# Kernel optimization log

Measured on AMD Instinct MI355X. Metric: run time of the kernel, lower is better.

## Reference

```python
import jax, jax.numpy as jnp
import numpy as np

INPUT_DIM = 2048
N_EXPERTS = 64
K = 2


def setup_inputs() -> dict:
    key = jax.random.key(0)
    kx, kw, kb = jax.random.split(key, 3)
    x = jax.random.normal(kx, (4, 4096, INPUT_DIM), dtype=jnp.float32)
    # nn.Linear(input_dim, n_experts): weight [n_experts, input_dim], bias [n_experts]
    bound = 1.0 / np.sqrt(INPUT_DIM)
    W = jax.random.uniform(kw, (N_EXPERTS, INPUT_DIM), minval=-bound, maxval=bound, dtype=jnp.float32)
    b = jax.random.uniform(kb, (N_EXPERTS,), minval=-bound, maxval=bound, dtype=jnp.float32)
    return {"x": x, "W": W, "b": b}


def reference(x, W, b):
    # logits: [B, S, E]
    logits = jnp.einsum('bsd,ed->bse', x, W) + b
    topk_vals, topk_indices = jax.lax.top_k(logits, K)  # over last (expert) axis
    gate_probs = jax.nn.softmax(topk_vals, axis=-1)
    return gate_probs, topk_indices
```

## Files before the change

kernel.cpp:

```cpp
#include <hip/hip_runtime.h>
#include <math.h>
#include <stdint.h>

typedef _Float16 half8 __attribute__((ext_vector_type(8)));
typedef float floatx4 __attribute__((ext_vector_type(4)));

#define NTOK   16384
#define DIM    2048
#define NEXP   64
#define TPB    16
#define NBLK   (NTOK / TPB)
#define NCHW   8
#define WSW_H8 16384
#define WSW_BYTES (2 * WSW_H8 * 16)

#define ABUF_BYTES 32768
#define RED_STRIDE 68
#define RED_F      (4 * 16 * RED_STRIDE)

__global__ void wprep_kernel(const float* __restrict__ W, _Float16* __restrict__ wsw) {
    const int id   = blockIdx.x * blockDim.x + threadIdx.x;
    const int lane = id & 63;
    const int tg   = (id >> 6) & 3;
    const int sg   = id >> 8;
    const int e    = tg * 16 + (lane & 15);
    const int k    = sg * 32 + (lane >> 4) * 8;
    const float* src = W + (size_t)e * DIM + k;
    half8 h, l;
#pragma unroll
    for (int j = 0; j < 8; j++) {
        const float v  = src[j];
        const _Float16 hh = (_Float16)v;
        h[j] = hh;
        l[j] = (_Float16)((v - (float)hh) * 2048.0f);
    }
    const size_t slot = (size_t)(sg * 4 + tg) * 64 + lane;
    ((half8*)wsw)[slot]          = h;
    ((half8*)wsw)[WSW_H8 + slot] = l;
}

__device__ __forceinline__ void split_a(const float4& v0, const float4& v1,
                                        half8& hi, half8& lo) {
    const float av[8] = {v0.x, v0.y, v0.z, v0.w, v1.x, v1.y, v1.z, v1.w};
#pragma unroll
    for (int j = 0; j < 8; j++) {
        const _Float16 hh = (_Float16)av[j];
        hi[j] = hh;
        lo[j] = (_Float16)((av[j] - (float)hh) * 2048.0f);
    }
}

__device__ __forceinline__ void dma16(const void* g, const char* l) {
    __builtin_amdgcn_global_load_lds(
        (const __attribute__((address_space(1))) unsigned int*)(uintptr_t)g,
        (__attribute__((address_space(3))) unsigned int*)(uintptr_t)l,
        16, 0, 0);
}

template <bool USE_WS> struct BFrag;
template <> struct BFrag<true>  { half8  h[2][4]; half8 l[2][4]; };
template <> struct BFrag<false> { float4 a[2][4][2]; };

template <bool USE_WS>
__device__ __forceinline__ void load_b(BFrag<USE_WS>& bf, const half8* wb,
                                       const float* Wb, int cc) {
    if constexpr (USE_WS) {
#pragma unroll
        for (int s = 0; s < 2; s++)
#pragma unroll
            for (int t = 0; t < 4; t++) {
                const size_t o = (size_t)(cc * 8 + s * 4 + t) * 64;
                bf.h[s][t] = wb[o];
                bf.l[s][t] = wb[o + WSW_H8];
            }
    } else {
#pragma unroll
        for (int s = 0; s < 2; s++)
#pragma unroll
            for (int t = 0; t < 4; t++) {
                const float* wr = Wb + (size_t)(t * 16) * DIM + cc * 64 + s * 32;
                bf.a[s][t][0] = *(const float4*)wr;
                bf.a[s][t][1] = *(const float4*)(wr + 4);
            }
    }
}

template <bool USE_WS>
__global__ __launch_bounds__(256, 3)
void gating_kernel(const float* __restrict__ x, const float* __restrict__ W,
                   const _Float16* __restrict__ wsw, const float* __restrict__ bias,
                   float* __restrict__ out)
{
    __shared__ char  abuf[ABUF_BYTES];
    __shared__ float red[RED_F];

    const int tid  = threadIdx.x;
    const int lane = tid & 63;
    const int ks   = tid >> 6;
    const int col  = lane & 15;
    const int quad = lane >> 4;
    const int tok0 = blockIdx.x * TPB;

    const float* gA[4];
#pragma unroll
    for (int i = 0; i < 4; i++) {
        const int row = i * 4 + quad;
        const int pz  = col;
        const int gp  = (pz & 8) | ((pz & 7) ^ (row & 7));
        gA[i] = x + (size_t)(tok0 + row) * DIM + ks * (NCHW * 64) + gp * 4;
    }
    char* const ab = abuf + ks * 8192;
    const half8* wb = (const half8*)wsw + (size_t)ks * 4096 + lane;
    const float* Wb = W + (size_t)col * DIM + ks * (NCHW * 64) + quad * 8;

    floatx4 accm[4] = {{0,0,0,0},{0,0,0,0},{0,0,0,0},{0,0,0,0}};
    floatx4 accl[4] = {{0,0,0,0},{0,0,0,0},{0,0,0,0},{0,0,0,0}};

#pragma unroll
    for (int i = 0; i < 4; i++) dma16(gA[i], ab + i * 1024);
    asm volatile("" ::: "memory");
    BFrag<USE_WS> bc;
    load_b<USE_WS>(bc, wb, Wb, 0);
#pragma unroll
    for (int i = 0; i < 4; i++) dma16(gA[i] + 64, ab + 4096 + i * 1024);

#pragma unroll
    for (int cc = 0; cc < NCHW; ++cc) {
        if (cc == NCHW - 1) asm volatile("s_waitcnt vmcnt(16)" ::: "memory");
        else                asm volatile("s_waitcnt vmcnt(20)" ::: "memory");
        const char* Ab = ab + (cc & 1) * 4096;
        float4 v0[2], v1[2];
#pragma unroll
        for (int s = 0; s < 2; s++) {
            v0[s] = *(const float4*)(Ab + col * 256 + (8 * s + ((2 * quad + 0) ^ (col & 7))) * 16);
            v1[s] = *(const float4*)(Ab + col * 256 + (8 * s + ((2 * quad + 1) ^ (col & 7))) * 16);
        }
        asm volatile("s_waitcnt lgkmcnt(0)" ::: "memory");
        BFrag<USE_WS> bn;
        if (cc + 1 < NCHW) load_b<USE_WS>(bn, wb, Wb, cc + 1);
        if (cc + 2 < NCHW) {
#pragma unroll
            for (int i = 0; i < 4; i++)
                dma16(gA[i] + (size_t)(cc + 2) * 64, ab + (cc & 1) * 4096 + i * 1024);
        }
#pragma unroll
        for (int s = 0; s < 2; s++) {
            half8 ah, al;
            split_a(v0[s], v1[s], ah, al);
#pragma unroll
            for (int t = 0; t < 4; t++) {
                half8 bh, bl;
                if constexpr (USE_WS) {
                    bh = bc.h[s][t];
                    bl = bc.l[s][t];
                } else {
                    split_a(bc.a[s][t][0], bc.a[s][t][1], bh, bl);
                }
                accm[t] = __builtin_amdgcn_mfma_f32_16x16x32_f16(ah, bh, accm[t], 0, 0, 0);
                accl[t] = __builtin_amdgcn_mfma_f32_16x16x32_f16(ah, bl, accl[t], 0, 0, 0);
                accl[t] = __builtin_amdgcn_mfma_f32_16x16x32_f16(al, bh, accl[t], 0, 0, 0);
            }
        }
        if (cc + 1 < NCHW) bc = bn;
    }

    const float inv = 1.0f / 2048.0f;
#pragma unroll
    for (int t = 0; t < 4; t++)
#pragma unroll
        for (int r = 0; r < 4; r++)
            red[(ks * 16 + quad * 4 + r) * RED_STRIDE + t * 16 + col] =
                accm[t][r] + accl[t][r] * inv;
    __syncthreads();

    if (tid < TPB) {
        const int tk = tid;
        float v0 = -INFINITY, v1 = -INFINITY;
        int   i0 = 0, i1 = 0;
        for (int e = 0; e < NEXP; e++) {
            const float v = red[(0 * 16 + tk) * RED_STRIDE + e]
                          + red[(1 * 16 + tk) * RED_STRIDE + e]
                          + red[(2 * 16 + tk) * RED_STRIDE + e]
                          + red[(3 * 16 + tk) * RED_STRIDE + e] + bias[e];
            if (v > v0)      { v1 = v0; i1 = i0; v0 = v; i0 = e; }
            else if (v > v1) { v1 = v; i1 = e; }
        }
        const float e1 = expf(v1 - v0);
        const float sden = 1.f + e1;
        const int   g  = tok0 + tk;
        out[2 * g + 0] = 1.f / sden;
        out[2 * g + 1] = e1 / sden;
        out[2 * NTOK + 2 * g + 0] = (float)i0;
        out[2 * NTOK + 2 * g + 1] = (float)i1;
    }
}

extern "C" void kernel_launch(void* const* d_in, const int* in_sizes, int n_in,
                              void* d_out, int out_size, void* d_ws, size_t ws_size,
                              hipStream_t stream) {
    const float* x    = (const float*)d_in[0];
    const float* W    = (const float*)d_in[1];
    const float* bias = (const float*)d_in[2];
    float*       out  = (float*)d_out;
    _Float16*    wsw  = (_Float16*)d_ws;

    if (ws_size >= (size_t)WSW_BYTES) {
        hipLaunchKernelGGL(wprep_kernel, dim3(64), dim3(256), 0, stream, W, wsw);
        hipLaunchKernelGGL((gating_kernel<true>), dim3(NBLK), dim3(256), 0, stream,
                           x, W, wsw, bias, out);
    } else {
        hipLaunchKernelGGL((gating_kernel<false>), dim3(NBLK), dim3(256), 0, stream,
                           x, W, wsw, bias, out);
    }
}
```

Baseline: 211.1 us.

## Process 64 tokens per block with 8-way K split to reuse weight fragments

```diff
diff --git a/kernel.cpp b/kernel.cpp
--- a/kernel.cpp
+++ b/kernel.cpp
@@ -5,18 +5,21 @@
 typedef _Float16 half8 __attribute__((ext_vector_type(8)));
 typedef float floatx4 __attribute__((ext_vector_type(4)));
 
-#define NTOK   16384
-#define DIM    2048
-#define NEXP   64
-#define TPB    16
-#define NBLK   (NTOK / TPB)
-#define NCHW   8
+#define NTOK 16384
+#define DIM  2048
+#define NEXP 64
+#define MB   64
+#define NBLK (NTOK / MB)
+#define KSPL 8
+#define KW   (DIM / KSPL)
+#define NCH  (KW / 32)
 #define WSW_H8 16384
 #define WSW_BYTES (2 * WSW_H8 * 16)
 
-#define ABUF_BYTES 32768
-#define RED_STRIDE 68
-#define RED_F      (4 * 16 * RED_STRIDE)
+#define SLOT_B  8192
+#define WAVE_B  (2 * SLOT_B)
+#define ARING_B (8 * WAVE_B)
+#define FIN_F   (64 * 65)
 
 __global__ void wprep_kernel(const float* __restrict__ W, _Float16* __restrict__ wsw) {
     const int id   = blockIdx.x * blockDim.x + threadIdx.x;
@@ -57,131 +60,134 @@
         16, 0, 0);
 }
 
-template <bool USE_WS> struct BFrag;
-template <> struct BFrag<true>  { half8  h[2][4]; half8 l[2][4]; };
-template <> struct BFrag<false> { float4 a[2][4][2]; };
+template <int N>
+__device__ __forceinline__ void wait_vm() {
+    asm volatile("s_waitcnt vmcnt(%0)" :: "n"(N) : "memory");
+}
 
 template <bool USE_WS>
-__device__ __forceinline__ void load_b(BFrag<USE_WS>& bf, const half8* wb,
-                                       const float* Wb, int cc) {
-    if constexpr (USE_WS) {
-#pragma unroll
-        for (int s = 0; s < 2; s++)
-#pragma unroll
-            for (int t = 0; t < 4; t++) {
-                const size_t o = (size_t)(cc * 8 + s * 4 + t) * 64;
-                bf.h[s][t] = wb[o];
-                bf.l[s][t] = wb[o + WSW_H8];
-            }
-    } else {
-#pragma unroll
-        for (int s = 0; s < 2; s++)
-#pragma unroll
-            for (int t = 0; t < 4; t++) {
-                const float* wr = Wb + (size_t)(t * 16) * DIM + cc * 64 + s * 32;
-                bf.a[s][t][0] = *(const float4*)wr;
-                bf.a[s][t][1] = *(const float4*)(wr + 4);
-            }
-    }
-}
-
-template <bool USE_WS>
-__global__ __launch_bounds__(256, 3)
+__global__ __launch_bounds__(512, 2)
 void gating_kernel(const float* __restrict__ x, const float* __restrict__ W,
                    const _Float16* __restrict__ wsw, const float* __restrict__ bias,
                    float* __restrict__ out)
 {
-    __shared__ char  abuf[ABUF_BYTES];
-    __shared__ float red[RED_F];
+    __shared__ char  aring[ARING_B];
+    __shared__ float fin[FIN_F];
+    __shared__ float bsh[NEXP];
 
     const int tid  = threadIdx.x;
     const int lane = tid & 63;
     const int ks   = tid >> 6;
     const int col  = lane & 15;
     const int quad = lane >> 4;
-    const int tok0 = blockIdx.x * TPB;
-
-    const float* gA[4];
-#pragma unroll
-    for (int i = 0; i < 4; i++) {
-        const int row = i * 4 + quad;
-        const int pz  = col;
-        const int gp  = (pz & 8) | ((pz & 7) ^ (row & 7));
-        gA[i] = x + (size_t)(tok0 + row) * DIM + ks * (NCHW * 64) + gp * 4;
-    }
-    char* const ab = abuf + ks * 8192;
-    const half8* wb = (const half8*)wsw + (size_t)ks * 4096 + lane;
-    const float* Wb = W + (size_t)col * DIM + ks * (NCHW * 64) + quad * 8;
-
-    floatx4 accm[4] = {{0,0,0,0},{0,0,0,0},{0,0,0,0},{0,0,0,0}};
-    floatx4 accl[4] = {{0,0,0,0},{0,0,0,0},{0,0,0,0},{0,0,0,0}};
-
-#pragma unroll
-    for (int i = 0; i < 4; i++) dma16(gA[i], ab + i * 1024);
-    asm volatile("" ::: "memory");
-    BFrag<USE_WS> bc;
-    load_b<USE_WS>(bc, wb, Wb, 0);
-#pragma unroll
-    for (int i = 0; i < 4; i++) dma16(gA[i] + 64, ab + 4096 + i * 1024);
-
-#pragma unroll
-    for (int cc = 0; cc < NCHW; ++cc) {
-        if (cc == NCHW - 1) asm volatile("s_waitcnt vmcnt(16)" ::: "memory");
-        else                asm volatile("s_waitcnt vmcnt(20)" ::: "memory");
-        const char* Ab = ab + (cc & 1) * 4096;
-        float4 v0[2], v1[2];
-#pragma unroll
-        for (int s = 0; s < 2; s++) {
-            v0[s] = *(const float4*)(Ab + col * 256 + (8 * s + ((2 * quad + 0) ^ (col & 7))) * 16);
-            v1[s] = *(const float4*)(Ab + col * 256 + (8 * s + ((2 * quad + 1) ^ (col & 7))) * 16);
-        }
-        asm volatile("s_waitcnt lgkmcnt(0)" ::: "memory");
-        BFrag<USE_WS> bn;
-        if (cc + 1 < NCHW) load_b<USE_WS>(bn, wb, Wb, cc + 1);
-        if (cc + 2 < NCHW) {
-#pragma unroll
-            for (int i = 0; i < 4; i++)
-                dma16(gA[i] + (size_t)(cc + 2) * 64, ab + (cc & 1) * 4096 + i * 1024);
-        }
-#pragma unroll
-        for (int s = 0; s < 2; s++) {
+    const int tok0 = blockIdx.x * MB;
+
+    if (tid < NEXP) bsh[tid] = bias[tid];
+
+    const int arow = lane >> 3;
+    const int agp  = (lane & 7) ^ arow;
+    const float* gA = x + (size_t)(tok0 + arow) * DIM + ks * KW + agp * 4;
+    char* const wbase = aring + ks * WAVE_B;
+
+    floatx4 accm[4][4], accl[4][4];
+#pragma unroll
+    for (int m = 0; m < 4; m++)
+#pragma unroll
+        for (int t = 0; t < 4; t++) { accm[m][t] = (floatx4){0,0,0,0}; accl[m][t] = (floatx4){0,0,0,0}; }
+
+#pragma unroll
+    for (int i = 0; i < 8; i++)
+        dma16(gA + (size_t)i * 8 * DIM, wbase + i * 1024);
+
+#pragma unroll
+    for (int c = 0; c < NCH; ++c) {
+        const int sg = ks * NCH + c;
+        half8  bh[4], bl[4];
+        float4 bf0[4], bf1[4];
+        if constexpr (USE_WS) {
+#pragma unroll
+            for (int t = 0; t < 4; t++) {
+                bh[t] = ((const half8*)wsw)[(size_t)(sg * 4 + t) * 64 + lane];
+                bl[t] = ((const half8*)wsw)[WSW_H8 + (size_t)(sg * 4 + t) * 64 + lane];
+            }
+        } else {
+#pragma unroll
+            for (int t = 0; t < 4; t++) {
+                const float* wr = W + (size_t)(t * 16 + col) * DIM + sg * 32 + quad * 8;
+                bf0[t] = *(const float4*)wr;
+                bf1[t] = *(const float4*)(wr + 4);
+            }
+        }
+        asm volatile("" ::: "memory");
+        if (c + 1 < NCH) {
+#pragma unroll
+            for (int i = 0; i < 8; i++)
+                dma16(gA + (size_t)i * 8 * DIM + (c + 1) * 32,
+                      wbase + ((c + 1) & 1) * SLOT_B + i * 1024);
+        }
+        asm volatile("" ::: "memory");
+        if (c + 1 < NCH) wait_vm<16>();
+        else             wait_vm<8>();
+        asm volatile("" ::: "memory");
+
+        const char* Ab = wbase + (c & 1) * SLOT_B;
+#pragma unroll
+        for (int m = 0; m < 4; m++) {
+            const int row = m * 16 + col;
+            const float4 v0 = *(const float4*)(Ab + row * 128 + (((2 * quad + 0) ^ (col & 7))) * 16);
+            const float4 v1 = *(const float4*)(Ab + row * 128 + (((2 * quad + 1) ^ (col & 7))) * 16);
             half8 ah, al;
-            split_a(v0[s], v1[s], ah, al);
+            split_a(v0, v1, ah, al);
 #pragma unroll
             for (int t = 0; t < 4; t++) {
-                half8 bh, bl;
-                if constexpr (USE_WS) {
-                    bh = bc.h[s][t];
-                    bl = bc.l[s][t];
-                } else {
-                    split_a(bc.a[s][t][0], bc.a[s][t][1], bh, bl);
-                }
-                accm[t] = __builtin_amdgcn_mfma_f32_16x16x32_f16(ah, bh, accm[t], 0, 0, 0);
-                accl[t] = __builtin_amdgcn_mfma_f32_16x16x32_f16(ah, bl, accl[t], 0, 0, 0);
-                accl[t] = __builtin_amdgcn_mfma_f32_16x16x32_f16(al, bh, accl[t], 0, 0, 0);
+                half8 hb, lb;
+                if constexpr (USE_WS) { hb = bh[t]; lb = bl[t]; }
+                else                  { split_a(bf0[t], bf1[t], hb, lb); }
+                accm[m][t] = __builtin_amdgcn_mfma_f32_16x16x32_f16(ah, hb, accm[m][t], 0, 0, 0);
+                accl[m][t] = __builtin_amdgcn_mfma_f32_16x16x32_f16(ah, lb, accl[m][t], 0, 0, 0);
+                accl[m][t] = __builtin_amdgcn_mfma_f32_16x16x32_f16(al, hb, accl[m][t], 0, 0, 0);
             }
         }
-        if (cc + 1 < NCHW) bc = bn;
-    }
-
-    const float inv = 1.0f / 2048.0f;
-#pragma unroll
-    for (int t = 0; t < 4; t++)
-#pragma unroll
-        for (int r = 0; r < 4; r++)
-            red[(ks * 16 + quad * 4 + r) * RED_STRIDE + t * 16 + col] =
-                accm[t][r] + accl[t][r] * inv;
+    }
+
     __syncthreads();
-
-    if (tid < TPB) {
+    {
+        float* slab = (float*)(aring + ks * 16384);
+        const float inv = 1.0f / 2048.0f;
+#pragma unroll
+        for (int m = 0; m < 4; m++)
+#pragma unroll
+            for (int t = 0; t < 4; t++)
+#pragma unroll
+                for (int r = 0; r < 4; r++)
+                    slab[(m * 16 + quad * 4 + r) * 64 + t * 16 + col] =
+                        accm[m][t][r] + accl[m][t][r] * inv;
+    }
+    __syncthreads();
+    {
+        const int tk = tid >> 3;
+        const int e0 = (tid & 7) * 8;
+        floatx4 s0 = {0,0,0,0}, s1 = {0,0,0,0};
+#pragma unroll
+        for (int p = 0; p < KSPL; p++) {
+            const float* sb = (const float*)(aring + p * 16384) + tk * 64 + e0;
+            s0 += *(const floatx4*)sb;
+            s1 += *(const floatx4*)(sb + 4);
+        }
+#pragma unroll
+        for (int j = 0; j < 4; j++) {
+            fin[tk * 65 + e0 + j]     = s0[j] + bsh[e0 + j];
+            fin[tk * 65 + e0 + 4 + j] = s1[j] + bsh[e0 + 4 + j];
+        }
+    }
+    __syncthreads();
+
+    if (tid < MB) {
         const int tk = tid;
         float v0 = -INFINITY, v1 = -INFINITY;
         int   i0 = 0, i1 = 0;
         for (int e = 0; e < NEXP; e++) {
-            const float v = red[(0 * 16 + tk) * RED_STRIDE + e]
-                          + red[(1 * 16 + tk) * RED_STRIDE + e]
-                          + red[(2 * 16 + tk) * RED_STRIDE + e]
-                          + red[(3 * 16 + tk) * RED_STRIDE + e] + bias[e];
+            const float v = fin[tk * 65 + e];
             if (v > v0)      { v1 = v0; i1 = i0; v0 = v; i0 = e; }
             else if (v > v1) { v1 = v; i1 = e; }
         }
@@ -206,10 +212,10 @@
 
     if (ws_size >= (size_t)WSW_BYTES) {
         hipLaunchKernelGGL(wprep_kernel, dim3(64), dim3(256), 0, stream, W, wsw);
-        hipLaunchKernelGGL((gating_kernel<true>), dim3(NBLK), dim3(256), 0, stream,
+        hipLaunchKernelGGL((gating_kernel<true>), dim3(NBLK), dim3(512), 0, stream,
                            x, W, wsw, bias, out);
     } else {
-        hipLaunchKernelGGL((gating_kernel<false>), dim3(NBLK), dim3(256), 0, stream,
-                           x, W, wsw, bias, out);
-    }
-}
+        hipLaunchKernelGGL((gating_kernel<false>), dim3(NBLK), dim3(512), 0, stream,
+                           x, W, nullptr, bias, out);
+    }
+}
```

Result: faster. 203.6 us (median of 2 runs) (-3.5%).
